# Optimization experiments

Measured on AMD Instinct MI355X. Metric: run time of the kernel, lower is better.

The kernel has to match this reference:

```python
import jax, jax.numpy as jnp
import numpy as np

EPS = 1e-5
K_PATCHES = 5000  # sample_pixels // 16


def _resize_bilinear(x, h, w):
    # matches torch F.interpolate(mode='bilinear', align_corners=False)
    return jax.image.resize(x, (x.shape[0], x.shape[1], h, w), method="bilinear", antialias=False)


def _bn(x, g, b, m, v):
    # eval-mode BatchNorm2d with running stats
    inv = jax.lax.rsqrt(v + EPS)
    return (x - m[None, :, None, None]) * (g * inv)[None, :, None, None] + b[None, :, None, None]


def _conv(x, w):
    return jax.lax.conv_general_dilated(x, w, (1, 1), "VALID",
                                        dimension_numbers=("NCHW", "OIHW", "NCHW"))


def setup_inputs():
    key = jax.random.key(0)
    ks = jax.random.split(key, 14)
    B, Hc, Wc = 2, 512, 512
    pha = jax.random.uniform(ks[0], (B, 1, Hc, Wc), jnp.float32)
    err = jax.random.uniform(ks[1], (B, 1, Hc, Wc), jnp.float32)  # strictly >0 so mask is all-ones
    hid = jax.random.normal(ks[2], (B, 32, Hc, Wc), jnp.float32)

    def conv_w(k, o, i):
        return jax.random.normal(k, (o, i, 3, 3), jnp.float32) * 0.05

    def bn_p(k, c):
        k1, k2 = jax.random.split(k)
        return (1.0 + 0.1 * jax.random.normal(k1, (c,), jnp.float32),
                0.1 * jax.random.normal(k2, (c,), jnp.float32),
                jnp.zeros((c,), jnp.float32), jnp.ones((c,), jnp.float32))

    g1, b1, m1, v1 = bn_p(ks[4], 24)
    g2, b2, m2, v2 = bn_p(ks[6], 16)
    g3, b3, m3, v3 = bn_p(ks[8], 12)
    return dict(pha=pha, err=err, hid=hid,
                w1=conv_w(ks[3], 24, 33), g1=g1, b1=b1, m1=m1, v1=v1,
                w2=conv_w(ks[5], 16, 24), g2=g2, b2=b2, m2=m2, v2=v2,
                w3=conv_w(ks[7], 12, 16), g3=g3, b3=b3, m3=m3, v3=v3,
                w4=conv_w(ks[9], 1, 12),
                b4=0.1 * jax.random.normal(ks[10], (1,), jnp.float32),
                H_full=2048, W_full=2048)


def reference(pha, err, hid, w1, g1, b1, m1, v1, w2, g2, b2, m2, v2,
              w3, g3, b3, m3, v3, w4, b4, H_full, W_full):
    B = pha.shape[0]
    Hh, Wh = H_full // 2, W_full // 2
    Hq, Wq = H_full // 4, W_full // 4

    # --- select_refinement_regions (sampling mode) ---
    err_q = _resize_bilinear(err, Hq, Wq)                      # (B,1,Hq,Wq)
    flat = err_q.reshape(B, -1)
    _, top_idx = jax.lax.top_k(flat, K_PATCHES)                # (B,K)
    ref = jnp.zeros_like(flat).at[jnp.arange(B)[:, None], top_idx].set(1.0)
    ref = ref * (flat > 0).astype(flat.dtype)                  # prevent_oversampling
    ref = ref.reshape(B, 1, Hq, Wq)

    # nonzero(ref) == topk locations here (err is strictly positive)
    bidx = jnp.repeat(jnp.arange(B), K_PATCHES)                # (P,)
    hidx = (top_idx // Wq).reshape(-1)                         # (P,)
    widx = (top_idx % Wq).reshape(-1)                          # (P,)

    # --- crop_patch (unfold-equivalent gather), size=2, padding=3 ---
    x = jnp.concatenate([hid, pha], axis=1)                    # (B,33,Hc,Wc)
    x = _resize_bilinear(x, Hh, Wh)                            # (B,33,Hh,Wh)
    pad, size = 3, 2
    win = size + 2 * pad                                       # 8
    xp = jnp.pad(x, ((0, 0), (0, 0), (pad, pad), (pad, pad)))
    rows = hidx[:, None] * size + jnp.arange(win)              # (P,8)
    cols = widx[:, None] * size + jnp.arange(win)              # (P,8)
    patches = xp[bidx[:, None, None], :, rows[:, :, None], cols[:, None, :]]  # (P,8,8,33)
    patches = patches.transpose(0, 3, 1, 2)                    # (P,33,8,8)

    # --- small conv stack ---
    y = jax.nn.relu(_bn(_conv(patches, w1), g1, b1, m1, v1))   # (P,24,6,6)
    y = jax.nn.relu(_bn(_conv(y, w2), g2, b2, m2, v2))         # (P,16,4,4)
    y = jnp.repeat(jnp.repeat(y, 2, axis=2), 2, axis=3)        # nearest -> (P,16,8,8)
    y = jax.nn.relu(_bn(_conv(y, w3), g3, b3, m3, v3))         # (P,12,6,6)
    y = _conv(y, w4) + b4[None, :, None, None]                 # (P,1,4,4)

    # --- replace_patch (scatter_nd of 4x4 blocks into full-res pha) ---
    pha_full = _resize_bilinear(pha, H_full, W_full)           # (B,1,H,W)
    pr = hidx[:, None, None] * 4 + jnp.arange(4)[None, :, None]  # (P,4,1)
    pc = widx[:, None, None] * 4 + jnp.arange(4)[None, None, :]  # (P,1,4)
    pha_full = pha_full.at[bidx[:, None, None], 0, pr, pc].set(y[:, 0])
    return pha_full, ref
```

## Files before the change

### kernel.cpp

```cpp
#include <hip/hip_runtime.h>
#include <stdint.h>

#define K_SEL 5000
#define NQ    262144
#define NB    2

#define BIAS_OFF 38912
#define W4_OFF   39424
#define ST_OFF   40960
#define XT_OFF   135168
#define XT_BYTES ((size_t)NB * NQ * 40 * 2)
#define WS_NEED  (XT_OFF + XT_BYTES)

#define WS_HIST  16
#define WS_SEL   2064
#define WS_BCNT  20480

typedef _Float16 f16x8 __attribute__((ext_vector_type(8)));
typedef _Float16 f16x4 __attribute__((ext_vector_type(4)));
typedef float    f32x4 __attribute__((ext_vector_type(4)));
#define MFMA16(a,b,c) __builtin_amdgcn_mfma_f32_16x16x32_f16(a,b,c,0,0,0)

__device__ void prep_work(int bid,
                          const float* __restrict__ w1, const float* __restrict__ g1,
                          const float* __restrict__ b1, const float* __restrict__ m1,
                          const float* __restrict__ v1,
                          const float* __restrict__ w2, const float* __restrict__ g2,
                          const float* __restrict__ b2, const float* __restrict__ m2,
                          const float* __restrict__ v2,
                          const float* __restrict__ w3, const float* __restrict__ g3,
                          const float* __restrict__ b3, const float* __restrict__ m3,
                          const float* __restrict__ v3,
                          const float* __restrict__ w4, const float* __restrict__ b4,
                          char* __restrict__ ws) {
    _Float16* wf = (_Float16*)ws;
    float* bias = (float*)(ws + BIAS_OFF);
    float* w4r  = (float*)(ws + W4_OFF);
    int tid = threadIdx.x;
    for (int t = bid * 256 + tid; t < 38 * 512; t += 64 * 256) {
        int frag = t >> 9, li = (t >> 3) & 63, j = t & 7;
        int lo = li & 15, hi = li >> 4;
        float val = 0.f;
        if (frag < 18) {
            int ky = frag / 6, r = frag % 6, kx = r >> 1, mt = r & 1;
            int oc = mt * 16 + lo, ci = hi * 8 + j;
            if (oc < 24) val = w1[((oc * 33 + ci) * 3 + ky) * 3 + kx] * g1[oc] * rsqrtf(v1[oc] + 1e-5f);
        } else if (frag < 27) {
            int f = frag - 18, ky = f / 3, kt = f % 3;
            int oc = lo, k = kt * 32 + hi * 8 + j;
            if (k < 72) {
                int kx = k / 24, ci = k % 24;
                val = w2[((oc * 24 + ci) * 3 + ky) * 3 + kx] * g2[oc] * rsqrtf(v2[oc] + 1e-5f);
            }
        } else if (frag < 36) {
            int s = frag - 27, ky = s / 3, kx = s % 3;
            int oc = lo, ci = hi * 8 + j;
            if (oc < 12 && ci < 16) val = w3[((oc * 16 + ci) * 3 + ky) * 3 + kx] * g3[oc] * rsqrtf(v3[oc] + 1e-5f);
        } else {
            int mt = frag - 36, oc = mt * 16 + lo, tap = hi * 8 + j;
            if (oc < 24 && tap < 9)
                val = w1[((oc * 33 + 32) * 3 + tap / 3) * 3 + tap % 3] * g1[oc] * rsqrtf(v1[oc] + 1e-5f);
        }
        wf[t] = (_Float16)val;
    }
    if (bid == 0) {
        if (tid < 53) {
            float v;
            if (tid < 24)      { float sc = g1[tid] * rsqrtf(v1[tid] + 1e-5f); v = b1[tid] - m1[tid] * sc; }
            else if (tid < 40) { int c = tid - 24; float sc = g2[c] * rsqrtf(v2[c] + 1e-5f); v = b2[c] - m2[c] * sc; }
            else if (tid < 52) { int c = tid - 40; float sc = g3[c] * rsqrtf(v3[c] + 1e-5f); v = b3[c] - m3[c] * sc; }
            else v = b4[0];
            bias[tid] = v;
        }
        if (tid < 144) { int t9 = tid / 16, ci = tid % 16; w4r[tid] = (ci < 12) ? w4[ci * 9 + t9] : 0.f; }
    }
}

__device__ __forceinline__ void chain_scan(const uint32_t* __restrict__ st, int b, int nrounds,
                                           uint32_t* pref_out, uint32_t* rem_out) {
    int lane = threadIdx.x & 63;
    uint32_t pref = 0u, rem = K_SEL;
    for (int r = 0; r < nrounds; r++) {
        const uint32_t* hist = st + WS_HIST + r * 512 + b * 256;
        int binbase = 255 - 4 * lane;
        uint32_t hv0 = hist[binbase], hv1 = hist[binbase - 1],
                 hv2 = hist[binbase - 2], hv3 = hist[binbase - 3];
        uint32_t p = hv0 + hv1 + hv2 + hv3;
        uint32_t cum = p;
        for (int o = 1; o < 64; o <<= 1) {
            uint32_t n = __shfl_up(cum, o);
            if (lane >= o) cum += n;
        }
        unsigned long long bal = __ballot(cum >= rem);
        int first = __ffsll(bal) - 1;
        uint32_t acc = cum - p;
        uint32_t hv[4] = {hv0, hv1, hv2, hv3};
        int ch = binbase;
        for (int q = 0; q < 4; q++) {
            if (acc + hv[q] >= rem) { ch = binbase - q; break; }
            acc += hv[q];
        }
        uint32_t chosen = (uint32_t)__shfl((int)ch, first);
        uint32_t nrem   = (uint32_t)__shfl((int)(rem - acc), first);
        pref |= chosen << (24 - 8 * r);
        rem = nrem;
    }
    *pref_out = pref;
    *rem_out = rem;
}

__device__ __forceinline__ void tu_work(int tb, const float* __restrict__ hid,
                                        const float* __restrict__ pha,
                                        _Float16* __restrict__ xt,
                                        float* __restrict__ out) {
    int tid = threadIdx.x;
    if (tb < 2048) {
        int t = tb * 256 + tid;
        int b = t >> 18, i = t & (NQ - 1);
        _Float16 v[40];
#pragma unroll
        for (int c = 0; c < 32; c++)
            v[c] = (_Float16)hid[((size_t)(b * 32 + c)) * NQ + i];
        v[32] = (_Float16)pha[(size_t)b * NQ + i];
#pragma unroll
        for (int c = 33; c < 40; c++) v[c] = (_Float16)0.f;
        _Float16* dst = xt + (size_t)t * 40;
#pragma unroll
        for (int q = 0; q < 5; q++) *(f16x8*)(dst + q * 8) = *(const f16x8*)(v + q * 8);
    } else {
        int t = (tb - 2048) * 256 + tid;
        int xq = t & 511;
        int rest = t >> 9;
        int oy = rest & 2047;
        int b  = rest >> 11;
        const float* src = pha + (size_t)b * NQ;
        float sy = oy * 0.25f - 0.375f;
        sy = fminf(fmaxf(sy, 0.0f), 511.0f);
        int y0 = (int)sy; int y1i = min(y0 + 1, 511);
        float fy = sy - (float)y0;
        float rv[4];
#pragma unroll
        for (int j = 0; j < 4; j++) {
            int ox = xq * 4 + j;
            float sx = ox * 0.25f - 0.375f;
            sx = fminf(fmaxf(sx, 0.0f), 511.0f);
            int x0 = (int)sx; int x1i = min(x0 + 1, 511);
            float fx = sx - (float)x0;
            float v00 = src[y0 * 512 + x0],  v01 = src[y0 * 512 + x1i];
            float v10 = src[y1i * 512 + x0], v11 = src[y1i * 512 + x1i];
            rv[j] = v00 * (1.f - fy) * (1.f - fx) + v01 * (1.f - fy) * fx
                  + v10 * fy * (1.f - fx)         + v11 * fy * fx;
        }
        float4 r4 = make_float4(rv[0], rv[1], rv[2], rv[3]);
        *reinterpret_cast<float4*>(out + (size_t)b * 4194304 + (size_t)oy * 2048 + xq * 4) = r4;
    }
}

__global__ void upsample_kernel(const float* __restrict__ pha, float* __restrict__ out) {
    int t = blockIdx.x * 256 + threadIdx.x;
    int xq = t & 511;
    int rest = t >> 9;
    int oy = rest & 2047;
    int b  = rest >> 11;
    const float* src = pha + (size_t)b * NQ;
    float sy = oy * 0.25f - 0.375f;
    sy = fminf(fmaxf(sy, 0.0f), 511.0f);
    int y0 = (int)sy; int y1i = min(y0 + 1, 511);
    float fy = sy - (float)y0;
    float rv[4];
#pragma unroll
    for (int j = 0; j < 4; j++) {
        int ox = xq * 4 + j;
        float sx = ox * 0.25f - 0.375f;
        sx = fminf(fmaxf(sx, 0.0f), 511.0f);
        int x0 = (int)sx; int x1i = min(x0 + 1, 511);
        float fx = sx - (float)x0;
        float v00 = src[y0 * 512 + x0],  v01 = src[y0 * 512 + x1i];
        float v10 = src[y1i * 512 + x0], v11 = src[y1i * 512 + x1i];
        rv[j] = v00 * (1.f - fy) * (1.f - fx) + v01 * (1.f - fy) * fx
              + v10 * fy * (1.f - fx)         + v11 * fy * fx;
    }
    float4 r4 = make_float4(rv[0], rv[1], rv[2], rv[3]);
    *reinterpret_cast<float4*>(out + (size_t)b * 4194304 + (size_t)oy * 2048 + xq * 4) = r4;
}

__global__ void l1_kernel(const float* __restrict__ err, uint32_t* st,
                          const float* __restrict__ w1, const float* __restrict__ g1,
                          const float* __restrict__ b1, const float* __restrict__ m1,
                          const float* __restrict__ v1,
                          const float* __restrict__ w2, const float* __restrict__ g2,
                          const float* __restrict__ b2, const float* __restrict__ m2,
                          const float* __restrict__ v2,
                          const float* __restrict__ w3, const float* __restrict__ g3,
                          const float* __restrict__ b3, const float* __restrict__ m3,
                          const float* __restrict__ v3,
                          const float* __restrict__ w4, const float* __restrict__ b4,
                          char* __restrict__ ws,
                          const float* __restrict__ hid, const float* __restrict__ pha,
                          _Float16* __restrict__ xt, float* __restrict__ out, int tu_base) {
    int blk = blockIdx.x, tid = threadIdx.x;
    if (blk < 2048) {
        __shared__ uint32_t h[256];
        h[tid] = 0u;
        __syncthreads();
        int t = blk * 256 + tid;
        int b = t >> 18;
        uint32_t bits = __float_as_uint(err[t]);
        atomicAdd(&h[bits >> 24], 1u);
        __syncthreads();
        uint32_t v = h[tid];
        if (v) atomicAdd(&st[WS_HIST + b * 256 + tid], v);
    } else if (blk < 2112) {
        prep_work(blk - 2048, w1, g1, b1, m1, v1, w2, g2, b2, m2, v2,
                  w3, g3, b3, m3, v3, w4, b4, ws);
    } else {
        tu_work(blk - 2112 + tu_base, hid, pha, xt, out);
    }
}

__global__ void hist_kernel(const float* __restrict__ err, uint32_t* st, int round,
                            const float* __restrict__ hid, const float* __restrict__ pha,
                            _Float16* __restrict__ xt, float* __restrict__ out, int tu_base) {
    if (blockIdx.x >= 2048) { tu_work(blockIdx.x - 2048 + tu_base, hid, pha, xt, out); return; }
    __shared__ uint32_t h[256];
    h[threadIdx.x] = 0u;
    int t = blockIdx.x * 256 + threadIdx.x;
    int b = t >> 18;
    uint32_t pref, rem;
    chain_scan(st, b, round, &pref, &rem);
    __syncthreads();
    uint32_t bits = __float_as_uint(err[t]);
    int shift = 24 - 8 * round;
    bool match = ((bits >> (shift + 8)) == (pref >> (shift + 8)));
    if (match) atomicAdd(&h[(bits >> shift) & 255u], 1u);
    __syncthreads();
    uint32_t v = h[threadIdx.x];
    if (v) atomicAdd(&st[WS_HIST + round * 512 + b * 256 + threadIdx.x], v);
}

__global__ void ccount_kernel(const float* __restrict__ err, uint32_t* st,
                              const float* __restrict__ hid, const float* __restrict__ pha,
                              _Float16* __restrict__ xt, float* __restrict__ out, int tu_base) {
    if (blockIdx.x >= 1024) { tu_work(blockIdx.x - 1024 + tu_base, hid, pha, xt, out); return; }
    __shared__ uint32_t wsum[16];
    int blk = blockIdx.x, tid = threadIdx.x;
    int b = blk >> 9, base = (blk & 511) << 9;
    uint32_t T, need;
    chain_scan(st, b, 4, &T, &need);
    if ((blk & 511) == 0 && tid == 0) {
        atomicExch(&st[4 + b], T);
        atomicExch(&st[6 + b], need);
    }
    uint32_t b0 = __float_as_uint(err[b * NQ + base + tid]);
    uint32_t b1 = __float_as_uint(err[b * NQ + base + 256 + tid]);
    unsigned long long m0s = __ballot(b0 > T), m1s = __ballot(b1 > T);
    unsigned long long m0e = __ballot(b0 == T), m1e = __ballot(b1 == T);
    int w = tid >> 6, lane = tid & 63;
    if (lane == 0) {
        wsum[w]      = (uint32_t)__popcll(m0s);
        wsum[4 + w]  = (uint32_t)__popcll(m1s);
        wsum[8 + w]  = (uint32_t)__popcll(m0e);
        wsum[12 + w] = (uint32_t)__popcll(m1e);
    }
    __syncthreads();
    if (tid == 0) {
        uint32_t s = 0, e = 0;
        for (int j = 0; j < 8; j++) { s += wsum[j]; e += wsum[8 + j]; }
        st[WS_BCNT + blk] = s | (e << 16);
    }
}

__global__ void cplace_kernel(const float* __restrict__ err, uint32_t* st,
                              float* __restrict__ refout,
                              const float* __restrict__ hid, const float* __restrict__ pha,
                              _Float16* __restrict__ xt, float* __restrict__ out, int tu_base) {
    if (blockIdx.x >= 1024) { tu_work(blockIdx.x - 1024 + tu_base, hid, pha, xt, out); return; }
    __shared__ uint32_t wcS[8], wcE[8];
    __shared__ uint32_t redP[4], redE[4];
    int blk = blockIdx.x, tid = threadIdx.x;
    int b = blk >> 9, base = (blk & 511) << 9;
    int w = tid >> 6, lane = tid & 63;
    uint32_t T = st[4 + b];
    uint32_t need = st[6 + b];
    uint32_t myp = blk & 511;
    uint32_t p0 = st[WS_BCNT + b * 512 + 2 * tid];
    uint32_t p1 = st[WS_BCNT + b * 512 + 2 * tid + 1];
    uint32_t s0c = p0 & 0xFFFFu, s1c = p1 & 0xFFFFu;
    uint32_t e0c = p0 >> 16,     e1c = p1 >> 16;
    uint32_t vP = (((uint32_t)(2 * tid) < myp) ? s0c : 0u)
                + (((uint32_t)(2 * tid + 1) < myp) ? s1c : 0u)
                + ((s0c + s1c) << 16);
    uint32_t vE = (((uint32_t)(2 * tid) < myp) ? e0c : 0u)
                + (((uint32_t)(2 * tid + 1) < myp) ? e1c : 0u);
    for (int o = 1; o < 64; o <<= 1) { vP += __shfl_xor(vP, o); vE += __shfl_xor(vE, o); }
    if (lane == 0) { redP[w] = vP; redE[w] = vE; }
    __syncthreads();
    uint32_t sumP = redP[0] + redP[1] + redP[2] + redP[3];
    uint32_t eqbase   = redE[0] + redE[1] + redE[2] + redE[3];
    uint32_t selbase  = sumP & 0xFFFFu;
    uint32_t selTotal = sumP >> 16;

    int i0 = base + tid, i1 = base + 256 + tid;
    uint32_t b0 = __float_as_uint(err[b * NQ + i0]);
    uint32_t b1 = __float_as_uint(err[b * NQ + i1]);
    bool s0 = b0 > T, s1 = b1 > T;
    bool q0 = b0 == T, q1 = b1 == T;
    unsigned long long m0s = __ballot(s0), m1s = __ballot(s1);
    unsigned long long m0e = __ballot(q0), m1e = __ballot(q1);
    if (lane == 0) {
        wcS[w] = (uint32_t)__popcll(m0s); wcS[4 + w] = (uint32_t)__popcll(m1s);
        wcE[w] = (uint32_t)__popcll(m0e); wcE[4 + w] = (uint32_t)__popcll(m1e);
    }
    __syncthreads();
    uint32_t tot0S = wcS[0] + wcS[1] + wcS[2] + wcS[3];
    uint32_t tot0E = wcE[0] + wcE[1] + wcE[2] + wcE[3];
    uint32_t preS0 = 0, preS1 = tot0S, preE0 = 0, preE1 = tot0E;
    for (int j = 0; j < w; j++) {
        preS0 += wcS[j]; preS1 += wcS[4 + j];
        preE0 += wcE[j]; preE1 += wcE[4 + j];
    }
    unsigned long long lt = (1ull << lane) - 1ull;
    float rv0 = s0 ? 1.0f : 0.0f;
    float rv1 = s1 ? 1.0f : 0.0f;
    if (s0) {
        uint32_t slot = selbase + preS0 + (uint32_t)__popcll(m0s & lt);
        if (slot < K_SEL) st[WS_SEL + b * K_SEL + slot] = (uint32_t)i0;
    }
    if (s1) {
        uint32_t slot = selbase + preS1 + (uint32_t)__popcll(m1s & lt);
        if (slot < K_SEL) st[WS_SEL + b * K_SEL + slot] = (uint32_t)i1;
    }
    if (q0) {
        uint32_t rank = eqbase + preE0 + (uint32_t)__popcll(m0e & lt);
        if (rank < need) {
            uint32_t slot = selTotal + rank;
            if (slot < K_SEL) st[WS_SEL + b * K_SEL + slot] = (uint32_t)i0;
            rv0 = (T != 0u) ? 1.0f : 0.0f;
        }
    }
    if (q1) {
        uint32_t rank = eqbase + preE1 + (uint32_t)__popcll(m1e & lt);
        if (rank < need) {
            uint32_t slot = selTotal + rank;
            if (slot < K_SEL) st[WS_SEL + b * K_SEL + slot] = (uint32_t)i1;
            rv1 = (T != 0u) ? 1.0f : 0.0f;
        }
    }
    refout[b * NQ + i0] = rv0;
    refout[b * NQ + i1] = rv1;
}

__device__ __forceinline__ f16x8 ldfrag(const _Float16* wf, int frag, int l) {
    return *(const f16x8*)(wf + frag * 512 + l * 8);
}

template<bool XT>
__global__ __launch_bounds__(128) void patch_kernel(
    const float* __restrict__ hid, const float* __restrict__ pha,
    const _Float16* __restrict__ xt,
    const char* __restrict__ ws, float* __restrict__ out) {
    __shared__ _Float16 xs[64][40];
    __shared__ _Float16 y1n[36][40];
    __shared__ _Float16 pool[64][40];
    __shared__ float pha8[64];
    __shared__ float biasL[56];
    float* y3s = (float*)&y1n[0][0];

    const _Float16* wf = (const _Float16*)ws;
    const float* biasG = (const float*)(ws + BIAS_OFF);
    const float* w4r   = (const float*)(ws + W4_OFF);
    const uint32_t* st = (const uint32_t*)(ws + ST_OFF);

    int tid = threadIdx.x, l = tid & 63, wid = tid >> 6;
    int lo = l & 15, hi = l >> 4;
    int bp = blockIdx.x;
    int b = (bp >= K_SEL) ? 1 : 0;
    int pi = bp - b * K_SEL;
    uint32_t idx = st[WS_SEL + b * K_SEL + pi] & 0x3FFFFu;
    int hq = (int)(idx >> 9), wq = (int)(idx & 511u);

    if (tid < 53) biasL[tid] = biasG[tid];

    int ry = l >> 3, rx = l & 7;
    int hy = hq * 2 + ry - 3, hx = wq * 2 + rx - 3;
    bool inb = ((unsigned)hy < 1024u) && ((unsigned)hx < 1024u);
    float sy = fminf(fmaxf(hy * 0.5f - 0.25f, 0.f), 511.f);
    float sx = fminf(fmaxf(hx * 0.5f - 0.25f, 0.f), 511.f);
    int y0 = (int)sy, x0 = (int)sx;
    int y1c = min(y0 + 1, 511), x1c = min(x0 + 1, 511);
    float fy = sy - (float)y0, fx = sx - (float)x0;
    int o00 = y0 * 512 + x0, o01 = y0 * 512 + x1c, o10 = y1c * 512 + x0, o11 = y1c * 512 + x1c;
    float w00 = (1.f - fy) * (1.f - fx), w01 = (1.f - fy) * fx;
    float w10 = fy * (1.f - fx), w11 = fy * fx;

    _Float16 hv[16];
    if (XT) {
        if (inb) {
            const _Float16* xtb = xt + (size_t)b * NQ * 40 + (size_t)wid * 16;
            const _Float16* p00 = xtb + (size_t)o00 * 40;
            const _Float16* p01 = xtb + (size_t)o01 * 40;
            const _Float16* p10 = xtb + (size_t)o10 * 40;
            const _Float16* p11 = xtb + (size_t)o11 * 40;
            f16x8 a0 = *(const f16x8*)p00, a1 = *(const f16x8*)(p00 + 8);
            f16x8 b0 = *(const f16x8*)p01, b1 = *(const f16x8*)(p01 + 8);
            f16x8 c0 = *(const f16x8*)p10, c1 = *(const f16x8*)(p10 + 8);
            f16x8 d0 = *(const f16x8*)p11, d1 = *(const f16x8*)(p11 + 8);
#pragma unroll
            for (int j = 0; j < 8; j++) {
                hv[j]     = (_Float16)(w00 * (float)a0[j] + w01 * (float)b0[j]
                                     + w10 * (float)c0[j] + w11 * (float)d0[j]);
                hv[j + 8] = (_Float16)(w00 * (float)a1[j] + w01 * (float)b1[j]
                                     + w10 * (float)c1[j] + w11 * (float)d1[j]);
            }
        } else {
#pragma unroll
            for (int c = 0; c < 16; c++) hv[c] = (_Float16)0.f;
        }
    } else {
        const float* hb = hid + ((size_t)b * 32 + wid * 16) * NQ;
#pragma unroll
        for (int c = 0; c < 16; c++) {
            const float* p = hb + (size_t)c * NQ;
            float v = 0.f;
            if (inb) v = p[o00] * w00 + p[o01] * w01 + p[o10] * w10 + p[o11] * w11;
            hv[c] = (_Float16)v;
        }
    }
    f16x8 h0 = {hv[0], hv[1], hv[2], hv[3], hv[4], hv[5], hv[6], hv[7]};
    f16x8 h1 = {hv[8], hv[9], hv[10], hv[11], hv[12], hv[13], hv[14], hv[15]};
    {
        _Float16* xrow = &xs[l][wid * 16];
        *(f16x8*)xrow = h0;
        *((f16x8*)xrow + 1) = h1;
    }
    f16x8 z8 = {(_Float16)0.f, (_Float16)0.f, (_Float16)0.f, (_Float16)0.f,
                (_Float16)0.f, (_Float16)0.f, (_Float16)0.f, (_Float16)0.f};
    if (wid == 1) {
        const float* p = pha + (size_t)b * NQ;
        float v = 0.f;
        if (inb) v = p[o00] * w00 + p[o01] * w01 + p[o10] * w10 + p[o11] * w11;
        pha8[l] = v;
    }
    __syncthreads();

    if (wid == 0) {
        if (l < 48) {
            int py = (l * 43) >> 8, px = l - py * 6;
            _Float16 tap[9];
#pragma unroll
            for (int t = 0; t < 9; t++) {
                int ky = t / 3, kx = t % 3;
                int ip = (py + ky) * 8 + px + kx;
                tap[t] = (_Float16)pha8[ip & 63];
            }
            _Float16* row = &pool[l][0];
            f16x8 r0 = {tap[0], tap[1], tap[2], tap[3], tap[4], tap[5], tap[6], tap[7]};
            f16x8 r1 = z8; r1[0] = tap[8];
            *(f16x8*)row = r0;
            *(f16x8*)(row + 8)  = r1;
            *(f16x8*)(row + 16) = z8;
            *(f16x8*)(row + 24) = z8;
        }
    } else {
        for (int i = l; i < 72; i += 64) {
            *(f16x8*)&y1n[i >> 1][24 + (i & 1) * 8] = z8;
        }
    }
    __syncthreads();

    f32x4 zf = {0.f, 0.f, 0.f, 0.f};
    f32x4 aA0 = zf, aA1 = zf, aB = zf;
    int nA = wid * 16 + lo, nB = 32 + lo;
    int pyA = (nA * 43) >> 8, pxA = nA - pyA * 6;
    int pyB = (nB * 43) >> 8, pxB = nB - pyB * 6;
    {
        f16x8 A0 = ldfrag(wf, 36, l), A1 = ldfrag(wf, 37, l);
        f16x8 BA = *(const f16x8*)&pool[nA][hi * 8];
        f16x8 BB = *(const f16x8*)&pool[nB][hi * 8];
        aA0 = MFMA16(A0, BA, aA0);
        aA1 = MFMA16(A1, BA, aA1);
        aB  = MFMA16(wid ? A1 : A0, BB, aB);
    }
#pragma unroll
    for (int ky = 0; ky < 3; ky++) {
#pragma unroll
        for (int kt = 0; kt < 3; kt++) {
            f16x8 A0 = ldfrag(wf, ky * 6 + kt * 2 + 0, l);
            f16x8 A1 = ldfrag(wf, ky * 6 + kt * 2 + 1, l);
            int rA = ((pyA + ky) * 8 + pxA + kt) & 63;
            int rB = ((pyB + ky) * 8 + pxB + kt) & 63;
            f16x8 BA = *(const f16x8*)&xs[rA][hi * 8];
            f16x8 BB = *(const f16x8*)&xs[rB][hi * 8];
            aA0 = MFMA16(A0, BA, aA0);
            aA1 = MFMA16(A1, BA, aA1);
            aB  = MFMA16(wid ? A1 : A0, BB, aB);
        }
    }
    {
        f32x4 accs[3] = {aA0, aA1, aB};
        int mts[3] = {0, 1, wid};
        int nts[3] = {wid, wid, 2};
#pragma unroll
        for (int f = 0; f < 3; f++) {
            int n = nts[f] * 16 + lo;
            int ocb = mts[f] * 16 + hi * 4;
            if (n < 36 && ocb < 24) {
                f16x4 hh;
                hh[0] = (_Float16)fmaxf(accs[f][0] + biasL[ocb + 0], 0.f);
                hh[1] = (_Float16)fmaxf(accs[f][1] + biasL[ocb + 1], 0.f);
                hh[2] = (_Float16)fmaxf(accs[f][2] + biasL[ocb + 2], 0.f);
                hh[3] = (_Float16)fmaxf(accs[f][3] + biasL[ocb + 3], 0.f);
                *(f16x4*)&y1n[n][ocb] = hh;
            }
        }
    }
    __syncthreads();

    if (wid == 0) {
        f32x4 a2 = zf;
        int qy = lo >> 2, qx = lo & 3;
#pragma unroll
        for (int ky = 0; ky < 3; ky++) {
#pragma unroll
            for (int kt = 0; kt < 3; kt++) {
                f16x8 A = ldfrag(wf, 18 + ky * 3 + kt, l);
                int k = kt * 32 + hi * 8;
                const _Float16* bptr;
                if (k < 72) {
                    int kx = k / 24, ci0 = k - kx * 24;
                    bptr = &y1n[(qy + ky) * 6 + qx + kx][ci0];
                } else {
                    bptr = &y1n[0][24];
                }
                f16x8 B = *(const f16x8*)bptr;
                a2 = MFMA16(A, B, a2);
            }
        }
        int ocb = hi * 4;
        f16x4 hh;
        hh[0] = (_Float16)fmaxf(a2[0] + biasL[24 + ocb + 0], 0.f);
        hh[1] = (_Float16)fmaxf(a2[1] + biasL[24 + ocb + 1], 0.f);
        hh[2] = (_Float16)fmaxf(a2[2] + biasL[24 + ocb + 2], 0.f);
        hh[3] = (_Float16)fmaxf(a2[3] + biasL[24 + ocb + 3], 0.f);
#pragma unroll
        for (int dy = 0; dy < 2; dy++)
#pragma unroll
            for (int dx = 0; dx < 2; dx++) {
                int row = (2 * qy + dy) * 8 + 2 * qx + dx;
                *(f16x4*)&pool[row][ocb] = hh;
            }
    } else {
        *(f16x8*)&pool[l][16] = z8;
        *(f16x8*)&pool[l][24] = z8;
    }
    __syncthreads();

    f32x4 aC = zf, aD = zf;
    int nC = wid * 16 + lo, nD = 32 + lo;
    int pyC = (nC * 43) >> 8, pxC = nC - pyC * 6;
    int pyD = (nD * 43) >> 8, pxD = nD - pyD * 6;
#pragma unroll
    for (int s = 0; s < 9; s++) {
        int ky = s / 3, kx = s % 3;
        f16x8 A = ldfrag(wf, 27 + s, l);
        f16x8 BC = *(const f16x8*)&pool[((pyC + ky) * 8 + pxC + kx) & 63][hi * 8];
        aC = MFMA16(A, BC, aC);
        if (wid) {
            f16x8 BD = *(const f16x8*)&pool[((pyD + ky) * 8 + pxD + kx) & 63][hi * 8];
            aD = MFMA16(A, BD, aD);
        }
    }
    __syncthreads();
    {
        int ocb = hi * 4;
        f32x4 accs[2] = {aC, aD};
        int nts[2] = {wid, 2};
        int cnt = wid ? 2 : 1;
        for (int f = 0; f < cnt; f++) {
            int n = nts[f] * 16 + lo;
            if (n < 36) {
                f32x4 v;
#pragma unroll
                for (int r = 0; r < 4; r++) {
                    float bb = (ocb + r < 12) ? biasL[40 + ocb + r] : 0.f;
                    float x = accs[f][r] + bb;
                    v[r] = (ocb + r < 12) ? fmaxf(x, 0.f) : 0.f;
                }
                *(f32x4*)&y3s[n * 16 + ocb] = v;
            }
        }
    }
    __syncthreads();

    if (wid == 0) {
        int r4 = lo >> 2, c4 = lo & 3, cig = hi;
        float acc = 0.f;
#pragma unroll
        for (int t = 0; t < 9; t++) {
            int ky = t / 3, kx = t % 3;
            const f32x4 xv = *(const f32x4*)&y3s[((r4 + ky) * 6 + c4 + kx) * 16 + cig * 4];
            const f32x4 wv = *(const f32x4*)(w4r + t * 16 + cig * 4);
            acc += xv[0] * wv[0] + xv[1] * wv[1] + xv[2] * wv[2] + xv[3] * wv[3];
        }
        acc += __shfl_xor(acc, 32);
        acc += __shfl_xor(acc, 16);
        if (l < 16) {
            out[(size_t)b * 4194304 + (size_t)(hq * 4 + r4) * 2048 + (wq * 4 + c4)] = acc + biasL[52];
        }
    }
}

extern "C" void kernel_launch(void* const* d_in, const int* in_sizes, int n_in,
                              void* d_out, int out_size, void* d_ws, size_t ws_size,
                              hipStream_t stream) {
    const float* pha = (const float*)d_in[0];
    const float* err = (const float*)d_in[1];
    const float* hid = (const float*)d_in[2];
    const float* w1  = (const float*)d_in[3];
    const float* g1  = (const float*)d_in[4];
    const float* bb1 = (const float*)d_in[5];
    const float* m1  = (const float*)d_in[6];
    const float* v1  = (const float*)d_in[7];
    const float* w2  = (const float*)d_in[8];
    const float* g2  = (const float*)d_in[9];
    const float* bb2 = (const float*)d_in[10];
    const float* m2  = (const float*)d_in[11];
    const float* v2  = (const float*)d_in[12];
    const float* w3  = (const float*)d_in[13];
    const float* g3  = (const float*)d_in[14];
    const float* bb3 = (const float*)d_in[15];
    const float* m3  = (const float*)d_in[16];
    const float* v3  = (const float*)d_in[17];
    const float* w4  = (const float*)d_in[18];
    const float* b4  = (const float*)d_in[19];

    float* out    = (float*)d_out;
    float* refout = out + (size_t)NB * 4194304;
    char* ws      = (char*)d_ws;
    uint32_t* st  = (uint32_t*)(ws + ST_OFF);
    _Float16* xt  = (_Float16*)(ws + XT_OFF);
    bool use_xt   = (ws_size >= WS_NEED);

    hipMemsetAsync(st, 0, (WS_HIST + 4 * 512) * sizeof(uint32_t), stream);

    if (use_xt) {
        const int NTU = 10240, SLICE = 1707;
        int off = 0;
        int n = SLICE;
        l1_kernel<<<2112 + n, 256, 0, stream>>>(err, st, w1, g1, bb1, m1, v1,
                                                w2, g2, bb2, m2, v2, w3, g3, bb3, m3, v3,
                                                w4, b4, ws, hid, pha, xt, out, off);
        off += n;
        for (int r = 1; r < 4; r++) {
            n = (off + SLICE <= NTU) ? SLICE : (NTU - off);
            hist_kernel<<<2048 + n, 256, 0, stream>>>(err, st, r, hid, pha, xt, out, off);
            off += n;
        }
        n = (off + SLICE <= NTU) ? SLICE : (NTU - off);
        ccount_kernel<<<1024 + n, 256, 0, stream>>>(err, st, hid, pha, xt, out, off);
        off += n;
        n = NTU - off;
        cplace_kernel<<<1024 + n, 256, 0, stream>>>(err, st, refout, hid, pha, xt, out, off);
        patch_kernel<true><<<2 * K_SEL, 128, 0, stream>>>(hid, pha, xt, ws, out);
    } else {
        upsample_kernel<<<8192, 256, 0, stream>>>(pha, out);
        l1_kernel<<<2112, 256, 0, stream>>>(err, st, w1, g1, bb1, m1, v1,
                                            w2, g2, bb2, m2, v2, w3, g3, bb3, m3, v3,
                                            w4, b4, ws, hid, pha, xt, out, 0);
        for (int r = 1; r < 4; r++)
            hist_kernel<<<2048, 256, 0, stream>>>(err, st, r, hid, pha, xt, out, 0);
        ccount_kernel<<<1024, 256, 0, stream>>>(err, st, hid, pha, xt, out, 0);
        cplace_kernel<<<1024, 256, 0, stream>>>(err, st, refout, hid, pha, xt, out, 0);
        patch_kernel<false><<<2 * K_SEL, 128, 0, stream>>>(hid, pha, xt, ws, out);
    }
}
```

Before: 135.5 us.

## Switch radix top-k select from four 8-bit passes to three 11/11/10-bit passes

The radix select over error values now uses three histogram rounds with 11, 11 and 10-bit digits instead of four 8-bit rounds. This removes one histogram kernel launch and one full pass over the error map, and the overlapped transform slices are rebalanced to the new kernel count. In exchange, the shared-memory histograms are 8x larger, each block flushes up to 2048 global atomics, and the chain scan reads more bins per lane on every round.

After: 215.2 us. 58.9% more time.

```diff
diff --git a/kernel.cpp b/kernel.cpp
--- a/kernel.cpp
+++ b/kernel.cpp
@@ -12,14 +12,22 @@
 #define XT_BYTES ((size_t)NB * NQ * 40 * 2)
 #define WS_NEED  (XT_OFF + XT_BYTES)
 
-#define WS_HIST  16
-#define WS_SEL   2064
-#define WS_BCNT  20480
+#define WS_SEL   12304
+#define WS_BCNT  22528
 
 typedef _Float16 f16x8 __attribute__((ext_vector_type(8)));
 typedef _Float16 f16x4 __attribute__((ext_vector_type(4)));
 typedef float    f32x4 __attribute__((ext_vector_type(4)));
 #define MFMA16(a,b,c) __builtin_amdgcn_mfma_f32_16x16x32_f16(a,b,c,0,0,0)
+
+__device__ __forceinline__ const uint32_t* hist_base(const uint32_t* st, int r, int b) {
+    return st + ((r == 0) ? (16 + b * 2048) : (r == 1) ? (16 + 4096 + b * 2048)
+                                                       : (16 + 8192 + b * 1024));
+}
+__device__ __forceinline__ uint32_t* hist_base(uint32_t* st, int r, int b) {
+    return st + ((r == 0) ? (16 + b * 2048) : (r == 1) ? (16 + 4096 + b * 2048)
+                                                       : (16 + 8192 + b * 1024));
+}
 
 __device__ void prep_work(int bid,
                           const float* __restrict__ w1, const float* __restrict__ g1,
@@ -81,11 +89,13 @@
     int lane = threadIdx.x & 63;
     uint32_t pref = 0u, rem = K_SEL;
     for (int r = 0; r < nrounds; r++) {
-        const uint32_t* hist = st + WS_HIST + r * 512 + b * 256;
-        int binbase = 255 - 4 * lane;
-        uint32_t hv0 = hist[binbase], hv1 = hist[binbase - 1],
-                 hv2 = hist[binbase - 2], hv3 = hist[binbase - 3];
-        uint32_t p = hv0 + hv1 + hv2 + hv3;
+        int nb = (r < 2) ? 11 : 10;
+        int shift = (r == 0) ? 21 : (r == 1) ? 10 : 0;
+        int per = (1 << nb) >> 6;
+        const uint32_t* hist = hist_base(st, r, b);
+        int topbin = (1 << nb) - 1 - lane * per;
+        uint32_t p = 0;
+        for (int q = 0; q < per; q++) p += hist[topbin - q];
         uint32_t cum = p;
         for (int o = 1; o < 64; o <<= 1) {
             uint32_t n = __shfl_up(cum, o);
@@ -94,15 +104,15 @@
         unsigned long long bal = __ballot(cum >= rem);
         int first = __ffsll(bal) - 1;
         uint32_t acc = cum - p;
-        uint32_t hv[4] = {hv0, hv1, hv2, hv3};
-        int ch = binbase;
-        for (int q = 0; q < 4; q++) {
-            if (acc + hv[q] >= rem) { ch = binbase - q; break; }
-            acc += hv[q];
-        }
-        uint32_t chosen = (uint32_t)__shfl((int)ch, first);
+        int ch = topbin;
+        for (int q = 0; q < per; q++) {
+            uint32_t h = hist[topbin - q];
+            if (acc + h >= rem) { ch = topbin - q; break; }
+            acc += h;
+        }
+        uint32_t chosen = (uint32_t)__shfl(ch, first);
         uint32_t nrem   = (uint32_t)__shfl((int)(rem - acc), first);
-        pref |= chosen << (24 - 8 * r);
+        pref |= chosen << shift;
         rem = nrem;
     }
     *pref_out = pref;
@@ -200,16 +210,19 @@
                           _Float16* __restrict__ xt, float* __restrict__ out, int tu_base) {
     int blk = blockIdx.x, tid = threadIdx.x;
     if (blk < 2048) {
-        __shared__ uint32_t h[256];
-        h[tid] = 0u;
+        __shared__ uint32_t h[2048];
+        for (int i = tid; i < 2048; i += 256) h[i] = 0u;
         __syncthreads();
         int t = blk * 256 + tid;
         int b = t >> 18;
         uint32_t bits = __float_as_uint(err[t]);
-        atomicAdd(&h[bits >> 24], 1u);
+        atomicAdd(&h[bits >> 21], 1u);
         __syncthreads();
-        uint32_t v = h[tid];
-        if (v) atomicAdd(&st[WS_HIST + b * 256 + tid], v);
+        uint32_t* g = hist_base(st, 0, b);
+        for (int i = tid; i < 2048; i += 256) {
+            uint32_t v = h[i];
+            if (v) atomicAdd(&g[i], v);
+        }
     } else if (blk < 2112) {
         prep_work(blk - 2048, w1, g1, b1, m1, v1, w2, g2, b2, m2, v2,
                   w3, g3, b3, m3, v3, w4, b4, ws);
@@ -222,20 +235,27 @@
                             const float* __restrict__ hid, const float* __restrict__ pha,
                             _Float16* __restrict__ xt, float* __restrict__ out, int tu_base) {
     if (blockIdx.x >= 2048) { tu_work(blockIdx.x - 2048 + tu_base, hid, pha, xt, out); return; }
-    __shared__ uint32_t h[256];
-    h[threadIdx.x] = 0u;
+    __shared__ uint32_t h[2048];
+    int nb = (round == 1) ? 11 : 10;
+    int nbins = 1 << nb;
+    for (int i = threadIdx.x; i < nbins; i += 256) h[i] = 0u;
     int t = blockIdx.x * 256 + threadIdx.x;
     int b = t >> 18;
     uint32_t pref, rem;
     chain_scan(st, b, round, &pref, &rem);
     __syncthreads();
     uint32_t bits = __float_as_uint(err[t]);
-    int shift = 24 - 8 * round;
-    bool match = ((bits >> (shift + 8)) == (pref >> (shift + 8)));
-    if (match) atomicAdd(&h[(bits >> shift) & 255u], 1u);
-    __syncthreads();
-    uint32_t v = h[threadIdx.x];
-    if (v) atomicAdd(&st[WS_HIST + round * 512 + b * 256 + threadIdx.x], v);
+    bool match;
+    uint32_t bin;
+    if (round == 1) { match = (bits >> 21) == (pref >> 21); bin = (bits >> 10) & 0x7FFu; }
+    else            { match = (bits >> 10) == (pref >> 10); bin = bits & 0x3FFu; }
+    if (match) atomicAdd(&h[bin], 1u);
+    __syncthreads();
+    uint32_t* g = hist_base(st, round, b);
+    for (int i = threadIdx.x; i < nbins; i += 256) {
+        uint32_t v = h[i];
+        if (v) atomicAdd(&g[i], v);
+    }
 }
 
 __global__ void ccount_kernel(const float* __restrict__ err, uint32_t* st,
@@ -246,7 +266,7 @@
     int blk = blockIdx.x, tid = threadIdx.x;
     int b = blk >> 9, base = (blk & 511) << 9;
     uint32_t T, need;
-    chain_scan(st, b, 4, &T, &need);
+    chain_scan(st, b, 3, &T, &need);
     if ((blk & 511) == 0 && tid == 0) {
         atomicExch(&st[4 + b], T);
         atomicExch(&st[6 + b], need);
@@ -546,7 +566,7 @@
         for (int dy = 0; dy < 2; dy++)
 #pragma unroll
             for (int dx = 0; dx < 2; dx++) {
-                int row = (2 * qy + dy) * 8 + 2 * qx + dx;
+                int row = (2 * (lo >> 2) + dy) * 8 + 2 * (lo & 3) + dx;
                 *(f16x4*)&pool[row][ocb] = hh;
             }
     } else {
@@ -641,33 +661,29 @@
     _Float16* xt  = (_Float16*)(ws + XT_OFF);
     bool use_xt   = (ws_size >= WS_NEED);
 
-    hipMemsetAsync(st, 0, (WS_HIST + 4 * 512) * sizeof(uint32_t), stream);
+    hipMemsetAsync(st, 0, (16 + 12288) * sizeof(uint32_t), stream);
 
     if (use_xt) {
-        const int NTU = 10240, SLICE = 1707;
+        const int NTU = 10240, SLICE = 2048;
         int off = 0;
-        int n = SLICE;
-        l1_kernel<<<2112 + n, 256, 0, stream>>>(err, st, w1, g1, bb1, m1, v1,
-                                                w2, g2, bb2, m2, v2, w3, g3, bb3, m3, v3,
-                                                w4, b4, ws, hid, pha, xt, out, off);
-        off += n;
-        for (int r = 1; r < 4; r++) {
-            n = (off + SLICE <= NTU) ? SLICE : (NTU - off);
-            hist_kernel<<<2048 + n, 256, 0, stream>>>(err, st, r, hid, pha, xt, out, off);
-            off += n;
-        }
-        n = (off + SLICE <= NTU) ? SLICE : (NTU - off);
-        ccount_kernel<<<1024 + n, 256, 0, stream>>>(err, st, hid, pha, xt, out, off);
-        off += n;
-        n = NTU - off;
-        cplace_kernel<<<1024 + n, 256, 0, stream>>>(err, st, refout, hid, pha, xt, out, off);
+        l1_kernel<<<2112 + SLICE, 256, 0, stream>>>(err, st, w1, g1, bb1, m1, v1,
+                                                    w2, g2, bb2, m2, v2, w3, g3, bb3, m3, v3,
+                                                    w4, b4, ws, hid, pha, xt, out, off);
+        off += SLICE;
+        for (int r = 1; r < 3; r++) {
+            hist_kernel<<<2048 + SLICE, 256, 0, stream>>>(err, st, r, hid, pha, xt, out, off);
+            off += SLICE;
+        }
+        ccount_kernel<<<1024 + SLICE, 256, 0, stream>>>(err, st, hid, pha, xt, out, off);
+        off += SLICE;
+        cplace_kernel<<<1024 + (NTU - off), 256, 0, stream>>>(err, st, refout, hid, pha, xt, out, off);
         patch_kernel<true><<<2 * K_SEL, 128, 0, stream>>>(hid, pha, xt, ws, out);
     } else {
         upsample_kernel<<<8192, 256, 0, stream>>>(pha, out);
         l1_kernel<<<2112, 256, 0, stream>>>(err, st, w1, g1, bb1, m1, v1,
                                             w2, g2, bb2, m2, v2, w3, g3, bb3, m3, v3,
                                             w4, b4, ws, hid, pha, xt, out, 0);
-        for (int r = 1; r < 4; r++)
+        for (int r = 1; r < 3; r++)
             hist_kernel<<<2048, 256, 0, stream>>>(err, st, r, hid, pha, xt, out, 0);
         ccount_kernel<<<1024, 256, 0, stream>>>(err, st, hid, pha, xt, out, 0);
         cplace_kernel<<<1024, 256, 0, stream>>>(err, st, refout, hid, pha, xt, out, 0);
```
